# Optimization experiments

Measured on AMD Instinct MI355X. Metric: run time of the kernel, lower is better.

## Reference

```python
import jax, jax.numpy as jnp
import numpy as np

B, T, H = 16, 512, 768
S = 32            # gold spans per example
L = 50            # max_span_len -> candidate ends per span
NT = 3            # num_types
HS = 4 * H        # span repr size


def setup_inputs() -> dict:
    key = jax.random.key(0)
    ks = jax.random.split(key, 8)
    h = jax.random.normal(ks[0], (B, T, H), dtype=jnp.float32)
    attention_mask = jnp.ones((B, T), dtype=jnp.int32)
    starts = jax.random.randint(ks[1], (B, S), 1, 400).astype(jnp.int32)
    lens = jax.random.randint(ks[2], (B, S), 0, L).astype(jnp.int32)
    ends = starts + lens                      # <= 448 < last_tok=510
    types = jax.random.randint(ks[3], (B, S), 0, NT).astype(jnp.int32)
    W1 = jax.random.normal(ks[4], (HS, HS), dtype=jnp.float32) * (1.0 / np.sqrt(HS))
    b1 = jnp.zeros((HS,), dtype=jnp.float32)
    w_score = jax.random.normal(ks[5], (HS,), dtype=jnp.float32) * (1.0 / np.sqrt(HS))
    b_score = jnp.zeros((1,), dtype=jnp.float32)
    W_type = jax.random.normal(ks[6], (HS, NT), dtype=jnp.float32) * (1.0 / np.sqrt(HS))
    b_type = jnp.zeros((NT,), dtype=jnp.float32)
    return {"h": h, "attention_mask": attention_mask, "span_starts": starts,
            "span_ends": ends, "span_types": types, "W1": W1, "b1": b1,
            "w_score": w_score, "b_score": b_score, "W_type": W_type, "b_type": b_type}


def _span_loss(h, attention_mask, span_starts, span_ends, span_types,
               W1, b1, w_score, b_score, W_type, b_type, type_loss_weight=1.0):
    cls = h[:, 0]                                              # [B,H]
    # prefix sums for O(1) segment means: pre[b,t] = sum h[b,0:t]
    pre = jnp.concatenate([jnp.zeros((B, 1, H), h.dtype), jnp.cumsum(h, axis=1)], axis=1)

    valid_len = attention_mask.sum(axis=1)                     # [B]
    last_tok = jnp.maximum(1, valid_len - 2)                   # [B]

    s = span_starts                                            # [B,S]
    e_gold = span_ends
    gold_idx = e_gold - s                                      # [B,S]
    lt = last_tok[:, None]
    span_valid = (s >= 1) & (s <= lt) & (e_gold >= s) & (e_gold <= lt) & (gold_idx < L)

    e_max = jnp.minimum(s + L - 1, lt)                         # [B,S]
    p = s[..., None] + jnp.arange(L, dtype=s.dtype)            # [B,S,L] candidate ends
    cand_valid = p <= e_max[..., None]

    sc = jnp.clip(s, 0, T - 1)
    pc = jnp.clip(p, 0, T - 1)
    bi2 = jnp.arange(B)[:, None]
    bi3 = jnp.arange(B)[:, None, None]

    h_start = h[bi2, sc]                                       # [B,S,H]
    h_end = h[bi3, pc]                                         # [B,S,L,H]
    seg_len = jnp.maximum(p - s[..., None] + 1, 1).astype(h.dtype)
    h_mean = (pre[bi3, pc + 1] - pre[bi2, sc][:, :, None]) / seg_len[..., None]

    repr_ = jnp.concatenate([
        jnp.broadcast_to(h_start[:, :, None], (B, S, L, H)),
        h_end,
        h_mean,
        jnp.broadcast_to(cls[:, None, None], (B, S, L, H)),
    ], axis=-1)                                                # [B,S,L,4H]

    h1 = jax.nn.gelu(jnp.einsum('bslh,hd->bsld', repr_, W1) + b1, approximate=False)
    scores = jnp.einsum('bsld,d->bsl', h1, w_score) + b_score[0]      # [B,S,L]
    type_logits = jnp.einsum('bsld,dk->bslk', h1, W_type) + b_type    # [B,S,L,NT]

    # end-index CE over valid candidate ends
    masked = jnp.where(cand_valid, scores, jnp.float32(-1e9))
    logp_end = jax.nn.log_softmax(masked, axis=-1)             # [B,S,L]
    gi = jnp.clip(gold_idx, 0, L - 1)
    end_loss = -jnp.take_along_axis(logp_end, gi[..., None], axis=-1)[..., 0]  # [B,S]

    # type CE at the gold end index
    tl_gold = jnp.take_along_axis(type_logits, gi[..., None, None], axis=2)[:, :, 0]  # [B,S,NT]
    logp_t = jax.nn.log_softmax(tl_gold, axis=-1)
    tg = jnp.clip(span_types, 0, NT - 1)
    type_loss = -jnp.take_along_axis(logp_t, tg[..., None], axis=-1)[..., 0]  # [B,S]

    vmask = span_valid.astype(h.dtype)
    n_seg = vmask.sum()
    denom = jnp.maximum(n_seg, 1.0)
    loss_end = jnp.where(n_seg > 0, (end_loss * vmask).sum() / denom, 0.0)
    loss_type = jnp.where(n_seg > 0, (type_loss * vmask).sum() / denom, 0.0)
    return loss_end + type_loss_weight * loss_type


def reference(h, attention_mask, span_starts, span_ends, span_types,
              W1, b1, w_score, b_score, W_type, b_type):
    return _span_loss(h, attention_mask, span_starts, span_ends, span_types,
                      W1, b1, w_score, b_score, W_type, b_type)
```

## Files before the change

### kernel.cpp

```cpp
#include <hip/hip_runtime.h>
#include <hip/hip_bf16.h>
#include <math.h>

#define B_ 16
#define T_ 512
#define H_ 768
#define S_ 32
#define L_ 50
#define NT_ 3
#define HS_ 3072
#define CH_ 32
#define CT_ 16

#define TX_ 464
#define YB2 7424
#define GB 14848
#define CLSB 15360
#define XYROWS 14848
#define AROWS 15616
#define NKT 24
#define SLOT_SH 16384
#define P1_BLOCKS (B_ * CH_ * 192 / 256)

typedef __attribute__((ext_vector_type(8))) short short8;
typedef __attribute__((ext_vector_type(4))) float f32x4;

__device__ __forceinline__ unsigned short f2bf(float f) {
    __hip_bfloat16 b = __float2bfloat16(f);
    return *(unsigned short*)&b;
}
__device__ __forceinline__ float bf2f(unsigned short u) {
    union { unsigned int i; float f; } v; v.i = ((unsigned int)u) << 16; return v.f;
}
__device__ __forceinline__ void load_lds16(const void* g, void* l) {
    __builtin_amdgcn_global_load_lds((__attribute__((address_space(1))) void*)g,
                                     (__attribute__((address_space(3))) void*)l, 16, 0, 0);
}
__device__ __forceinline__ ushort4 pack4(float4 v) {
    ushort4 o; o.x = f2bf(v.x); o.y = f2bf(v.y); o.z = f2bf(v.z); o.w = f2bf(v.w);
    return o;
}

__device__ __forceinline__ float gelu_exact(float v) {
    float a = fabsf(v) * 0.70710678118654752f;
    float t = __builtin_amdgcn_rcpf(fmaf(a, 0.47047f, 1.0f));
    float poly = t * fmaf(t, fmaf(t, 0.7478556f, -0.0958798f), 0.3480242f);
    float e = __builtin_amdgcn_exp2f(a * a * -1.4426950408889634f);
    float erfa = fmaf(-poly, e, 1.0f);
    float erfv = copysignf(erfa, v);
    return 0.5f * v * (1.0f + erfv);
}

__global__ __launch_bounds__(256) void prep_kernel(const float4* __restrict__ h4,
                                                   float4* __restrict__ partial,
                                                   const float* __restrict__ W1,
                                                   __hip_bfloat16* __restrict__ Wt) {
    __shared__ float tile[64][65];
    if (blockIdx.x < P1_BLOCKS) {
        int idx = blockIdx.x * 256 + threadIdx.x;
        int hd4 = idx % 192; int t = idx / 192; int ch = t % CH_; int b = t / CH_;
        const float4* hp = h4 + ((size_t)b * T_ + ch * CT_) * 192 + hd4;
        float4 acc = {0.f, 0.f, 0.f, 0.f};
#pragma unroll
        for (int tt = 0; tt < CT_; tt++) {
            float4 v = hp[(size_t)tt * 192];
            acc.x += v.x; acc.y += v.y; acc.z += v.z; acc.w += v.w;
        }
        partial[idx] = acc;
        return;
    }
    int bx = blockIdx.x - P1_BLOCKS;
    int n0 = (bx % 48) * 64, k0 = (bx / 48) * 64;
    int c = threadIdx.x & 63, r0 = threadIdx.x >> 6;
#pragma unroll
    for (int i = 0; i < 16; i++) {
        int r = r0 + i * 4;
        tile[r][c] = W1[(size_t)(k0 + r) * HS_ + n0 + c];
    }
    __syncthreads();
    int p = k0 / H_, kl = k0 % H_;
    __hip_bfloat16* out = Wt + (size_t)p * HS_ * H_;
#pragma unroll
    for (int i = 0; i < 16; i++) {
        int r = r0 + i * 4;
        out[(size_t)(n0 + r) * H_ + kl + c] = __float2bfloat16(tile[c][r]);
    }
}

__global__ __launch_bounds__(256) void cumsum_pass3(const float4* __restrict__ h4,
                                                    const float4* __restrict__ partial,
                                                    ushort4* __restrict__ Ab4,
                                                    const float* __restrict__ h,
                                                    const int* __restrict__ starts) {
    if (blockIdx.x >= P1_BLOCKS) {
        int r = blockIdx.x - P1_BLOCKS;
        int src_row, dst_row;
        if (r < B_ * S_) {
            int b = r / S_;
            int sv = starts[r];
            int sc = min(max(sv, 0), T_ - 1);
            src_row = b * T_ + sc;
            dst_row = GB + r;
        } else {
            int b = r - B_ * S_;
            src_row = b * T_;
            dst_row = CLSB + b;
        }
        __hip_bfloat16* dst = (__hip_bfloat16*)Ab4 + (size_t)dst_row * H_;
        const float* src = h + (size_t)src_row * H_;
        for (int j = threadIdx.x; j < H_; j += 256)
            dst[j] = __float2bfloat16(src[j]);
        return;
    }
    int idx = blockIdx.x * 256 + threadIdx.x;
    int hd4 = idx % 192; int t = idx / 192; int ch = t % CH_; int b = t / CH_;
    if (ch * CT_ >= TX_) return;
    float4 acc = {0.f, 0.f, 0.f, 0.f};
#pragma unroll
    for (int c = 0; c < CH_; c++) {
        if (c < ch) {
            float4 v = partial[((size_t)b * CH_ + c) * 192 + hd4];
            acc.x += v.x; acc.y += v.y; acc.z += v.z; acc.w += v.w;
        }
    }
    const float4* hp = h4 + ((size_t)b * T_ + ch * CT_) * 192 + hd4;
    if (ch == 0) {
        ushort4 z = {0, 0, 0, 0};
        Ab4[((size_t)(YB2 + b * TX_)) * 192 + hd4] = z;
    }
#pragma unroll
    for (int tt = 0; tt < CT_; tt++) {
        int t2 = ch * CT_ + tt;
        float4 hv = hp[(size_t)tt * 192];
        if (t2 < TX_)
            Ab4[((size_t)(b * TX_ + t2)) * 192 + hd4] = pack4(hv);
        acc.x += hv.x; acc.y += hv.y; acc.z += hv.z; acc.w += hv.w;
        if (t2 + 1 < TX_)
            Ab4[((size_t)(YB2 + b * TX_ + t2 + 1)) * 192 + hd4] = pack4(acc);
    }
}

__device__ __forceinline__ void mfma16(const short8 (&a)[4], const short8 (&b)[4],
                                       f32x4 (&acc)[8][4], int off) {
#pragma unroll
    for (int mf = 0; mf < 4; ++mf)
#pragma unroll
        for (int nf = 0; nf < 4; ++nf)
            acc[off + mf][nf] = __builtin_amdgcn_mfma_f32_16x16x32_bf16(
                a[mf], b[nf], acc[off + mf][nf], 0, 0, 0);
}

#define STAGE_A(nslot, k0_) {                                                  \
    char* d_ = (char*)(nslot) + dstoff;                                        \
    load_lds16(pA + (k0_), d_);                                                \
    load_lds16(pA + (size_t)128 * H_ + (k0_), d_ + 8192);                      \
}
#define STAGE_B(nslot, k0_) {                                                  \
    char* d_ = (char*)(nslot) + 16384 + dstoff;                                \
    load_lds16(pB + (k0_), d_);                                                \
    load_lds16(pB + (size_t)128 * H_ + (k0_), d_ + 8192);                      \
}

#define TILE_STEP(kt, WAITSTR, DO_STAGE)                                       \
  {                                                                            \
    const short* slot = lds + ((kt) & 3) * SLOT_SH;                            \
    short* nslot = lds + (((kt) + 3) & 3) * SLOT_SH;                           \
    asm volatile(WAITSTR ::: "memory");                                        \
    __builtin_amdgcn_s_barrier();                                              \
    __builtin_amdgcn_sched_barrier(0);                                         \
    short8 a[4], b[4];                                                         \
    _Pragma("unroll")                                                          \
    for (int i = 0; i < 4; ++i)                                                \
      a[i] = *(const short8*)&slot[(wr * 128 + i * 16 + l15) * 32 + pcs];      \
    _Pragma("unroll")                                                          \
    for (int i = 0; i < 4; ++i)                                                \
      b[i] = *(const short8*)&slot[8192 + (wc * 64 + i * 16 + l15) * 32 + pcs];\
    if (DO_STAGE) { STAGE_A(nslot, ((kt) + 3) * 32) }                          \
    asm volatile("s_waitcnt lgkmcnt(0)" ::: "memory");                         \
    __builtin_amdgcn_sched_barrier(0);                                         \
    __builtin_amdgcn_s_setprio(1);                                             \
    mfma16(a, b, acc, 0);                                                      \
    __builtin_amdgcn_s_setprio(0);                                             \
    __builtin_amdgcn_s_barrier();                                              \
    _Pragma("unroll")                                                          \
    for (int i = 0; i < 4; ++i)                                                \
      a[i] = *(const short8*)&slot[(wr * 128 + 64 + i * 16 + l15) * 32 + pcs]; \
    if (DO_STAGE) { STAGE_B(nslot, ((kt) + 3) * 32) }                          \
    asm volatile("s_waitcnt lgkmcnt(0)" ::: "memory");                         \
    __builtin_amdgcn_sched_barrier(0);                                         \
    __builtin_amdgcn_s_setprio(1);                                             \
    mfma16(a, b, acc, 4);                                                      \
    __builtin_amdgcn_s_setprio(0);                                             \
  }

__global__ __launch_bounds__(512, 2) void mfma_gemm(const __hip_bfloat16* __restrict__ Ab,
                                                    const __hip_bfloat16* __restrict__ Wt,
                                                    __hip_bfloat16* __restrict__ XY,
                                                    float* __restrict__ ST,
                                                    float* __restrict__ CC) {
    __shared__ short lds[4 * SLOT_SH];
    int tid = threadIdx.x;
    int wave = tid >> 6, lane = tid & 63;
    int wr = wave >> 2, wc = wave & 3;
    int l15 = lane & 15;
    int pcs = ((lane >> 4) ^ ((l15 >> 1) & 3)) * 8;

    int orig = blockIdx.x;
    int xcd = orig & 7, loc = orig >> 3;
    int wg = (xcd < 4 ? xcd * 92 : 368 + (xcd - 4) * 91) + loc;
    int mt = wg / 12, nt = wg - mt * 12;
    int m0 = mt << 8, n0 = nt << 8;

    const __hip_bfloat16* Bt;
    if (m0 < YB2)        Bt = Wt + (size_t)1 * HS_ * H_;
    else if (m0 < GB)    Bt = Wt + (size_t)2 * HS_ * H_;
    else if (m0 < CLSB)  Bt = Wt;
    else                 Bt = Wt + (size_t)3 * HS_ * H_;

    int srow = wave * 16 + (lane >> 2);
    int lcS = ((lane & 3) ^ ((lane >> 3) & 3)) * 8;
    const __hip_bfloat16* pA = Ab + (size_t)(m0 + srow) * H_ + lcS;
    const __hip_bfloat16* pB = Bt + (size_t)(n0 + srow) * H_ + lcS;
    int dstoff = wave * 1024;

    f32x4 acc[8][4] = {};

#pragma unroll
    for (int t = 0; t < 3; ++t) {
        STAGE_A(lds + t * SLOT_SH, t * 32)
        STAGE_B(lds + t * SLOT_SH, t * 32)
    }

    for (int kt = 0; kt < NKT - 3; ++kt)
        TILE_STEP(kt, "s_waitcnt vmcnt(8)", true)
    TILE_STEP(NKT - 3, "s_waitcnt vmcnt(8)", false)
    TILE_STEP(NKT - 2, "s_waitcnt vmcnt(4)", false)
    TILE_STEP(NKT - 1, "s_waitcnt vmcnt(0)", false)

    int mb = m0 + wr * 128, nb = n0 + wc * 64;
#pragma unroll
    for (int mf = 0; mf < 8; ++mf) {
#pragma unroll
        for (int nf = 0; nf < 4; ++nf) {
            int n = nb + nf * 16 + l15;
            int mr = mb + mf * 16 + (lane >> 4) * 4;
#pragma unroll
            for (int r = 0; r < 4; ++r) {
                int m = mr + r;
                float v = acc[mf][nf][r];
                if (m < XYROWS) {
                    XY[(size_t)m * HS_ + n] = __float2bfloat16(v);
                } else if (m < CLSB) {
                    ST[(size_t)(m - GB) * HS_ + n] = v;
                } else if (m < CLSB + 16) {
                    CC[(size_t)(m - CLSB) * HS_ + n] = v;
                }
            }
        }
    }
}

__global__ __launch_bounds__(512, 4) void combine_kernel(
    const float* __restrict__ ST, const float* __restrict__ CC,
    const float* __restrict__ b1, const float* __restrict__ w_score,
    const __hip_bfloat16* __restrict__ XY,
    const float* __restrict__ b_score, const float* __restrict__ W_type,
    const int* __restrict__ starts, const int* __restrict__ ends,
    float* __restrict__ scores, float* __restrict__ tgold) {
    __shared__ unsigned short ysL[HS_];
    __shared__ unsigned short cvL[HS_];
    __shared__ unsigned short wvL[HS_];
    int x = blockIdx.x;
    int b = x & 15, s = x >> 4;
    int bs = b * S_ + s;
    int tid = threadIdx.x;
    int wave = tid >> 6, lane = tid & 63;
    int sv = starts[bs], ev = ends[bs];
    int gi = min(max(ev - sv, 0), L_ - 1);
    int sc = min(max(sv, 0), TX_ - 1);
    float bs0 = b_score[0];

    const unsigned short* Ysr = (const unsigned short*)(XY + (size_t)(YB2 + b * TX_ + sc) * HS_);
    const float* STr = ST + (size_t)bs * HS_;
    const float* CCr = CC + (size_t)b * HS_;
    union U8 { short8 s; unsigned short u[8]; };
    for (int d = tid * 8; d < HS_; d += 512 * 8) {
        *(short8*)&ysL[d] = *(const short8*)(Ysr + d);
        float4 sa = *(const float4*)(STr + d), sb = *(const float4*)(STr + d + 4);
        float4 ca = *(const float4*)(CCr + d), cb = *(const float4*)(CCr + d + 4);
        float4 ba = *(const float4*)(b1 + d),  bb = *(const float4*)(b1 + d + 4);
        U8 uc;
        uc.u[0] = f2bf(sa.x + ca.x + ba.x); uc.u[1] = f2bf(sa.y + ca.y + ba.y);
        uc.u[2] = f2bf(sa.z + ca.z + ba.z); uc.u[3] = f2bf(sa.w + ca.w + ba.w);
        uc.u[4] = f2bf(sb.x + cb.x + bb.x); uc.u[5] = f2bf(sb.y + cb.y + bb.y);
        uc.u[6] = f2bf(sb.z + cb.z + bb.z); uc.u[7] = f2bf(sb.w + cb.w + bb.w);
        *(short8*)&cvL[d] = uc.s;
        float4 wa = *(const float4*)(w_score + d), wb = *(const float4*)(w_score + d + 4);
        U8 uw;
        uw.u[0] = f2bf(wa.x); uw.u[1] = f2bf(wa.y); uw.u[2] = f2bf(wa.z); uw.u[3] = f2bf(wa.w);
        uw.u[4] = f2bf(wb.x); uw.u[5] = f2bf(wb.y); uw.u[6] = f2bf(wb.z); uw.u[7] = f2bf(wb.w);
        *(short8*)&wvL[d] = uw.s;
    }
    __syncthreads();

    for (int pr = wave; pr < L_ / 2; pr += 8) {
        int l0 = pr * 2, l1 = l0 + 1;
        int pc0 = min(max(sv + l0, 0), TX_ - 2);
        int pc1 = min(max(sv + l1, 0), TX_ - 2);
        float inv0 = 1.0f / (float)(l0 + 1);
        float inv1 = 1.0f / (float)(l1 + 1);
        bool isg0 = (l0 == gi), isg1 = (l1 == gi);
        bool anyg = isg0 || isg1;

        const unsigned short* X0 = (const unsigned short*)(XY + (size_t)(b * TX_ + pc0) * HS_);
        const unsigned short* X1 = (const unsigned short*)(XY + (size_t)(b * TX_ + pc1) * HS_);
        const unsigned short* Y0 = (const unsigned short*)(XY + (size_t)(YB2 + b * TX_ + pc0 + 1) * HS_);
        const unsigned short* Y1 = (const unsigned short*)(XY + (size_t)(YB2 + b * TX_ + pc1 + 1) * HS_);

        float local0 = 0.f, local1 = 0.f, t0 = 0.f, t1 = 0.f, t2 = 0.f;
#pragma unroll 2
        for (int j = 0; j < 6; j++) {
            int d = j * 512 + lane * 8;
            short8 xv0 = *(const short8*)(X0 + d);
            short8 xv1 = *(const short8*)(X1 + d);
            short8 yv0 = *(const short8*)(Y0 + d);
            short8 yv1 = *(const short8*)(Y1 + d);
            short8 ys8 = *(const short8*)&ysL[d];
            short8 cv8 = *(const short8*)&cvL[d];
            short8 wv8 = *(const short8*)&wvL[d];
#pragma unroll
            for (int q = 0; q < 8; q++) {
                float ys = bf2f(((const unsigned short*)&ys8)[q]);
                float cvq = bf2f(((const unsigned short*)&cv8)[q]);
                float w  = bf2f(((const unsigned short*)&wv8)[q]);
                float v0 = fmaf(bf2f(((const unsigned short*)&yv0)[q]) - ys, inv0, cvq) +
                           bf2f(((const unsigned short*)&xv0)[q]);
                float v1 = fmaf(bf2f(((const unsigned short*)&yv1)[q]) - ys, inv1, cvq) +
                           bf2f(((const unsigned short*)&xv1)[q]);
                float g0 = gelu_exact(v0);
                float g1 = gelu_exact(v1);
                local0 = fmaf(g0, w, local0);
                local1 = fmaf(g1, w, local1);
                if (anyg) {
                    float gg = isg0 ? g0 : g1;
                    t0 = fmaf(gg, W_type[(d + q) * NT_ + 0], t0);
                    t1 = fmaf(gg, W_type[(d + q) * NT_ + 1], t1);
                    t2 = fmaf(gg, W_type[(d + q) * NT_ + 2], t2);
                }
            }
        }
#pragma unroll
        for (int off = 32; off >= 1; off >>= 1) {
            local0 += __shfl_down(local0, off);
            local1 += __shfl_down(local1, off);
        }
        if (lane == 0) {
            scores[(size_t)bs * L_ + l0] = local0 + bs0;
            scores[(size_t)bs * L_ + l1] = local1 + bs0;
        }
        if (anyg) {
#pragma unroll
            for (int off = 32; off >= 1; off >>= 1) {
                t0 += __shfl_down(t0, off);
                t1 += __shfl_down(t1, off);
                t2 += __shfl_down(t2, off);
            }
            if (lane == 0) {
                tgold[bs * NT_ + 0] = t0;
                tgold[bs * NT_ + 1] = t1;
                tgold[bs * NT_ + 2] = t2;
            }
        }
    }
}

__global__ __launch_bounds__(512) void loss_kernel(
    const float* __restrict__ scores, const float* __restrict__ tgold,
    const int* __restrict__ mask, const int* __restrict__ starts,
    const int* __restrict__ ends, const int* __restrict__ types,
    const float* __restrict__ b_type, float* __restrict__ out) {
    __shared__ int svl[B_];
    __shared__ float r[3][8];
    int tid = threadIdx.x;
    int b = tid / S_;
    if (tid < B_) svl[tid] = 0;
    __syncthreads();
    {
        int part = 0;
        const int* mp = mask + tid * 16;
#pragma unroll
        for (int i = 0; i < 16; i++) part += mp[i];
        atomicAdd(&svl[tid / (T_ / 16)], part);
    }
    __syncthreads();
    int vl = svl[b];
    int lt = max(1, vl - 2);
    int sv = starts[tid], ev = ends[tid];
    int gold = ev - sv;
    bool valid = (sv >= 1) && (sv <= lt) && (ev >= sv) && (ev <= lt) && (gold < L_);
    int emax = min(sv + L_ - 1, lt);
    const float* sp = scores + (size_t)tid * L_;
    float m = -1e30f;
    for (int l = 0; l < L_; l++) {
        float v = (sv + l <= emax) ? sp[l] : -1e9f;
        m = fmaxf(m, v);
    }
    float sum = 0.f;
    for (int l = 0; l < L_; l++) {
        float v = (sv + l <= emax) ? sp[l] : -1e9f;
        sum += expf(v - m);
    }
    int gi = min(max(gold, 0), L_ - 1);
    float vg = (sv + gi <= emax) ? sp[gi] : -1e9f;
    float end_loss = (m + logf(sum)) - vg;

    float t0 = tgold[tid * 3 + 0] + b_type[0];
    float t1 = tgold[tid * 3 + 1] + b_type[1];
    float t2 = tgold[tid * 3 + 2] + b_type[2];
    float tm = fmaxf(t0, fmaxf(t1, t2));
    float tsum = expf(t0 - tm) + expf(t1 - tm) + expf(t2 - tm);
    int tg = min(max(types[tid], 0), NT_ - 1);
    float tv = (tg == 0) ? t0 : ((tg == 1) ? t1 : t2);
    float type_loss = (tm + logf(tsum)) - tv;

    float ve = valid ? end_loss : 0.f;
    float vt = valid ? type_loss : 0.f;
    float vc = valid ? 1.f : 0.f;
    for (int off = 32; off >= 1; off >>= 1) {
        ve += __shfl_down(ve, off);
        vt += __shfl_down(vt, off);
        vc += __shfl_down(vc, off);
    }
    if ((tid & 63) == 0) {
        int w = tid >> 6;
        r[0][w] = ve; r[1][w] = vt; r[2][w] = vc;
    }
    __syncthreads();
    if (tid == 0) {
        float se = 0, st = 0, n = 0;
        for (int w = 0; w < 8; w++) { se += r[0][w]; st += r[1][w]; n += r[2][w]; }
        float denom = fmaxf(n, 1.f);
        out[0] = (n > 0.f) ? (se / denom + st / denom) : 0.f;
    }
}

extern "C" void kernel_launch(void* const* d_in, const int* in_sizes, int n_in,
                              void* d_out, int out_size, void* d_ws, size_t ws_size,
                              hipStream_t stream) {
    const float* h       = (const float*)d_in[0];
    const int*   mask    = (const int*)d_in[1];
    const int*   starts  = (const int*)d_in[2];
    const int*   ends    = (const int*)d_in[3];
    const int*   types   = (const int*)d_in[4];
    const float* W1      = (const float*)d_in[5];
    const float* b1      = (const float*)d_in[6];
    const float* w_score = (const float*)d_in[7];
    const float* b_score = (const float*)d_in[8];
    const float* W_type  = (const float*)d_in[9];
    const float* b_type  = (const float*)d_in[10];
    float* out = (float*)d_out;

    char* ws = (char*)d_ws;
    size_t off = 0;
    __hip_bfloat16* Ab = (__hip_bfloat16*)(ws + off); off += (size_t)AROWS * H_ * 2;
    __hip_bfloat16* XY = (__hip_bfloat16*)(ws + off); off += (size_t)XYROWS * HS_ * 2;
    __hip_bfloat16* Wt = (__hip_bfloat16*)(ws + off); off += (size_t)4 * HS_ * H_ * 2;
    float* ST     = (float*)(ws + off);               off += (size_t)512 * HS_ * 4;
    float* CC     = (float*)(ws + off);               off += (size_t)16 * HS_ * 4;
    float* scores = (float*)(ws + off);               off += (size_t)B_ * S_ * L_ * 4;
    float* tgold  = (float*)(ws + off);               off += (size_t)B_ * S_ * NT_ * 4;
    float4* partial = (float4*)XY;

    hipLaunchKernelGGL(prep_kernel, dim3(P1_BLOCKS + 48 * 48), dim3(256), 0, stream,
                       (const float4*)h, partial, W1, Wt);
    hipLaunchKernelGGL(cumsum_pass3, dim3(P1_BLOCKS + B_ * S_ + B_), dim3(256),
                       0, stream, (const float4*)h, (const float4*)partial, (ushort4*)Ab,
                       h, starts);
    hipLaunchKernelGGL(mfma_gemm, dim3((AROWS / 256) * 12), dim3(512), 0, stream,
                       Ab, Wt, XY, ST, CC);
    hipLaunchKernelGGL(combine_kernel, dim3(B_ * S_), dim3(512), 0, stream,
                       ST, CC, b1, w_score, XY, b_score, W_type, starts, ends,
                       scores, tgold);
    hipLaunchKernelGGL(loss_kernel, dim3(1), dim3(512), 0, stream,
                       scores, tgold, mask, starts, ends, types, b_type, out);
}
```

Before: 307.4 us.

## Fuse prefix-sum and gather into prep kernel with serial per-column scan

Replaces the two-pass chunked prefix sum (partial sums, then a second kernel) with a single sequential per-column scan inside the prep kernel. The W1 transpose and the start/CLS row gathers run in the same launch. This removes one kernel launch and the partial-sum round trip through memory. In exchange, only 48 blocks do a 464-step dependent loop, which reduces parallelism and may lengthen the critical path.

```diff
diff --git a/kernel.cpp b/kernel.cpp
--- a/kernel.cpp
+++ b/kernel.cpp
@@ -9,8 +9,6 @@
 #define L_ 50
 #define NT_ 3
 #define HS_ 3072
-#define CH_ 32
-#define CT_ 16
 
 #define TX_ 464
 #define YB2 7424
@@ -20,7 +18,8 @@
 #define AROWS 15616
 #define NKT 24
 #define SLOT_SH 16384
-#define P1_BLOCKS (B_ * CH_ * 192 / 256)
+#define CSB_ 48
+#define TRB_ (48 * 48)
 
 typedef __attribute__((ext_vector_type(8))) short short8;
 typedef __attribute__((ext_vector_type(4))) float f32x4;
@@ -35,10 +34,6 @@
 __device__ __forceinline__ void load_lds16(const void* g, void* l) {
     __builtin_amdgcn_global_load_lds((__attribute__((address_space(1))) void*)g,
                                      (__attribute__((address_space(3))) void*)l, 16, 0, 0);
-}
-__device__ __forceinline__ ushort4 pack4(float4 v) {
-    ushort4 o; o.x = f2bf(v.x); o.y = f2bf(v.y); o.z = f2bf(v.z); o.w = f2bf(v.w);
-    return o;
 }
 
 __device__ __forceinline__ float gelu_exact(float v) {
@@ -51,93 +46,66 @@
     return 0.5f * v * (1.0f + erfv);
 }
 
-__global__ __launch_bounds__(256) void prep_kernel(const float4* __restrict__ h4,
-                                                   float4* __restrict__ partial,
+__global__ __launch_bounds__(256) void prep_kernel(const float* __restrict__ h,
                                                    const float* __restrict__ W1,
-                                                   __hip_bfloat16* __restrict__ Wt) {
+                                                   __hip_bfloat16* __restrict__ Ab,
+                                                   __hip_bfloat16* __restrict__ Wt,
+                                                   const int* __restrict__ starts) {
     __shared__ float tile[64][65];
-    if (blockIdx.x < P1_BLOCKS) {
-        int idx = blockIdx.x * 256 + threadIdx.x;
-        int hd4 = idx % 192; int t = idx / 192; int ch = t % CH_; int b = t / CH_;
-        const float4* hp = h4 + ((size_t)b * T_ + ch * CT_) * 192 + hd4;
-        float4 acc = {0.f, 0.f, 0.f, 0.f};
-#pragma unroll
-        for (int tt = 0; tt < CT_; tt++) {
-            float4 v = hp[(size_t)tt * 192];
-            acc.x += v.x; acc.y += v.y; acc.z += v.z; acc.w += v.w;
-        }
-        partial[idx] = acc;
+    int tid = threadIdx.x;
+    if (blockIdx.x < CSB_) {
+        int b = blockIdx.x / 3, cg = blockIdx.x % 3;
+        int j = cg * 256 + tid;
+        const float* hp = h + (size_t)b * T_ * H_ + j;
+        __hip_bfloat16* hb = Ab + (size_t)(b * TX_) * H_ + j;
+        __hip_bfloat16* pb = Ab + (size_t)(YB2 + b * TX_) * H_ + j;
+        pb[0] = __float2bfloat16(0.0f);
+        float acc = 0.f;
+        for (int t = 0; t < TX_; ++t) {
+            float v = hp[(size_t)t * H_];
+            hb[(size_t)t * H_] = __float2bfloat16(v);
+            acc += v;
+            if (t + 1 < TX_)
+                pb[(size_t)(t + 1) * H_] = __float2bfloat16(acc);
+        }
         return;
     }
-    int bx = blockIdx.x - P1_BLOCKS;
-    int n0 = (bx % 48) * 64, k0 = (bx / 48) * 64;
-    int c = threadIdx.x & 63, r0 = threadIdx.x >> 6;
-#pragma unroll
-    for (int i = 0; i < 16; i++) {
-        int r = r0 + i * 4;
-        tile[r][c] = W1[(size_t)(k0 + r) * HS_ + n0 + c];
-    }
-    __syncthreads();
-    int p = k0 / H_, kl = k0 % H_;
-    __hip_bfloat16* out = Wt + (size_t)p * HS_ * H_;
-#pragma unroll
-    for (int i = 0; i < 16; i++) {
-        int r = r0 + i * 4;
-        out[(size_t)(n0 + r) * H_ + kl + c] = __float2bfloat16(tile[c][r]);
-    }
-}
-
-__global__ __launch_bounds__(256) void cumsum_pass3(const float4* __restrict__ h4,
-                                                    const float4* __restrict__ partial,
-                                                    ushort4* __restrict__ Ab4,
-                                                    const float* __restrict__ h,
-                                                    const int* __restrict__ starts) {
-    if (blockIdx.x >= P1_BLOCKS) {
-        int r = blockIdx.x - P1_BLOCKS;
-        int src_row, dst_row;
-        if (r < B_ * S_) {
-            int b = r / S_;
-            int sv = starts[r];
-            int sc = min(max(sv, 0), T_ - 1);
-            src_row = b * T_ + sc;
-            dst_row = GB + r;
-        } else {
-            int b = r - B_ * S_;
-            src_row = b * T_;
-            dst_row = CLSB + b;
-        }
-        __hip_bfloat16* dst = (__hip_bfloat16*)Ab4 + (size_t)dst_row * H_;
-        const float* src = h + (size_t)src_row * H_;
-        for (int j = threadIdx.x; j < H_; j += 256)
-            dst[j] = __float2bfloat16(src[j]);
+    if (blockIdx.x < CSB_ + TRB_) {
+        int bx = blockIdx.x - CSB_;
+        int n0 = (bx % 48) * 64, k0 = (bx / 48) * 64;
+        int c = tid & 63, r0 = tid >> 6;
+#pragma unroll
+        for (int i = 0; i < 16; i++) {
+            int r = r0 + i * 4;
+            tile[r][c] = W1[(size_t)(k0 + r) * HS_ + n0 + c];
+        }
+        __syncthreads();
+        int p = k0 / H_, kl = k0 % H_;
+        __hip_bfloat16* out = Wt + (size_t)p * HS_ * H_;
+#pragma unroll
+        for (int i = 0; i < 16; i++) {
+            int r = r0 + i * 4;
+            out[(size_t)(n0 + r) * H_ + kl + c] = __float2bfloat16(tile[c][r]);
+        }
         return;
     }
-    int idx = blockIdx.x * 256 + threadIdx.x;
-    int hd4 = idx % 192; int t = idx / 192; int ch = t % CH_; int b = t / CH_;
-    if (ch * CT_ >= TX_) return;
-    float4 acc = {0.f, 0.f, 0.f, 0.f};
-#pragma unroll
-    for (int c = 0; c < CH_; c++) {
-        if (c < ch) {
-            float4 v = partial[((size_t)b * CH_ + c) * 192 + hd4];
-            acc.x += v.x; acc.y += v.y; acc.z += v.z; acc.w += v.w;
-        }
-    }
-    const float4* hp = h4 + ((size_t)b * T_ + ch * CT_) * 192 + hd4;
-    if (ch == 0) {
-        ushort4 z = {0, 0, 0, 0};
-        Ab4[((size_t)(YB2 + b * TX_)) * 192 + hd4] = z;
-    }
-#pragma unroll
-    for (int tt = 0; tt < CT_; tt++) {
-        int t2 = ch * CT_ + tt;
-        float4 hv = hp[(size_t)tt * 192];
-        if (t2 < TX_)
-            Ab4[((size_t)(b * TX_ + t2)) * 192 + hd4] = pack4(hv);
-        acc.x += hv.x; acc.y += hv.y; acc.z += hv.z; acc.w += hv.w;
-        if (t2 + 1 < TX_)
-            Ab4[((size_t)(YB2 + b * TX_ + t2 + 1)) * 192 + hd4] = pack4(acc);
-    }
+    int r = blockIdx.x - CSB_ - TRB_;
+    int src_row, dst_row;
+    if (r < B_ * S_) {
+        int b = r / S_;
+        int sv = starts[r];
+        int sc = min(max(sv, 0), T_ - 1);
+        src_row = b * T_ + sc;
+        dst_row = GB + r;
+    } else {
+        int b = r - B_ * S_;
+        src_row = b * T_;
+        dst_row = CLSB + b;
+    }
+    __hip_bfloat16* dst = Ab + (size_t)dst_row * H_;
+    const float* src = h + (size_t)src_row * H_;
+    for (int jj = tid; jj < H_; jj += 256)
+        dst[jj] = __float2bfloat16(src[jj]);
 }
 
 __device__ __forceinline__ void mfma16(const short8 (&a)[4], const short8 (&b)[4],
@@ -469,13 +437,9 @@
     float* CC     = (float*)(ws + off);               off += (size_t)16 * HS_ * 4;
     float* scores = (float*)(ws + off);               off += (size_t)B_ * S_ * L_ * 4;
     float* tgold  = (float*)(ws + off);               off += (size_t)B_ * S_ * NT_ * 4;
-    float4* partial = (float4*)XY;
-
-    hipLaunchKernelGGL(prep_kernel, dim3(P1_BLOCKS + 48 * 48), dim3(256), 0, stream,
-                       (const float4*)h, partial, W1, Wt);
-    hipLaunchKernelGGL(cumsum_pass3, dim3(P1_BLOCKS + B_ * S_ + B_), dim3(256),
-                       0, stream, (const float4*)h, (const float4*)partial, (ushort4*)Ab,
-                       h, starts);
+
+    hipLaunchKernelGGL(prep_kernel, dim3(CSB_ + TRB_ + B_ * S_ + B_), dim3(256), 0, stream,
+                       h, W1, Ab, Wt, starts);
     hipLaunchKernelGGL(mfma_gemm, dim3((AROWS / 256) * 12), dim3(512), 0, stream,
                        Ab, Wt, XY, ST, CC);
     hipLaunchKernelGGL(combine_kernel, dim3(B_ * S_), dim3(512), 0, stream,
```

Result: slower. 460.4 us (+49.8%).
